# Kernel tuning notes

Hardware: AMD Instinct MI355X
Metric: run time of the kernel (lower is better)

The kernel has to match this reference:

```python
import jax, jax.numpy as jnp
import numpy as np

B, T, D, K = 8, 2048, 768, 2048

def setup_inputs() -> dict:
    key = jax.random.key(0)
    k1, k2 = jax.random.split(key)
    token = jax.random.normal(k1, (B, T, D), dtype=jnp.float32)
    codebook = jax.random.normal(k2, (K, D), dtype=jnp.float32)
    return {"token": token, "codebook": codebook}

def reference(token, codebook):
    x_sq = jnp.sum(token * token, axis=-1, keepdims=True)          # [B,T,1]
    e_sq = jnp.sum(codebook * codebook, axis=-1)                   # [K]
    dots = jnp.einsum('btd,kd->btk', token, codebook)              # [B,T,K]
    dist = x_sq - 2.0 * dots + e_sq                                # [B,T,K]
    indices = jnp.argmin(dist, axis=-1)                            # [B,T] int
    quantize = codebook[indices]                                   # [B,T,D] gather
    # commitment loss: mse(sg(quantize), x)
    commit_loss = jnp.mean(jnp.square(jax.lax.stop_gradient(quantize) - token))
    # straight-through estimator
    quantized = token + jax.lax.stop_gradient(quantize - token)
    return quantized, indices, commit_loss
```

## Files before the change

kernel.cpp:

```cpp
#include <hip/hip_runtime.h>

#define M_TOK 16384
#define D_DIM 768
#define K_CB  2048

#define BTOK  128
#define BCODE 128
#define BK    32
#define KSPLIT 8
#define SLICE (K_CB / KSPLIT)
#define NCT   (SLICE / BCODE)
#define NSLOT (KSPLIT * 2)
#define EPS   0.25f

typedef __attribute__((ext_vector_type(8))) short bf16x8;
typedef __attribute__((ext_vector_type(4))) float f32x4;

__device__ __forceinline__ unsigned short f2bf(float x) {
    unsigned u = __float_as_uint(x);
    return (unsigned short)((u + 0x7fffu + ((u >> 16) & 1u)) >> 16);
}
__device__ __forceinline__ float bf2f(unsigned short h) {
    return __uint_as_float((unsigned)h << 16);
}

#define ASYNC16(gp, lp) __builtin_amdgcn_global_load_lds( \
    (const __attribute__((address_space(1))) void*)(gp),  \
    (__attribute__((address_space(3))) void*)(lp), 16, 0, 0)

__global__ void vq_prep_cb(const float* __restrict__ cb,
                           unsigned short* __restrict__ cb_hi,
                           unsigned short* __restrict__ cb_lo,
                           float* __restrict__ esq) {
    const int w = threadIdx.x >> 6, lane = threadIdx.x & 63;
    const int k = blockIdx.x * 4 + w;
    const float* row = cb + (size_t)k * D_DIM;
    unsigned short* hk = cb_hi + (size_t)k * D_DIM;
    unsigned short* lk = cb_lo + (size_t)k * D_DIM;
    float s = 0.f;
    for (int j = lane; j < D_DIM; j += 64) {
        float x = row[j];
        s = fmaf(x, x, s);
        unsigned short h = f2bf(x);
        hk[j] = h;
        lk[j] = f2bf(x - bf2f(h));
    }
    #pragma unroll
    for (int off = 32; off; off >>= 1) s += __shfl_down(s, off);
    if (!lane) esq[k] = s;
}

__global__ void vq_prep_tok(const float* __restrict__ tok,
                            unsigned short* __restrict__ th,
                            unsigned short* __restrict__ tl) {
    const int N8 = (M_TOK * D_DIM) / 8;
    const int stride = gridDim.x * blockDim.x;
    for (int i = blockIdx.x * blockDim.x + threadIdx.x; i < N8; i += stride) {
        const float4 a = *(const float4*)(tok + (size_t)i * 8);
        const float4 b = *(const float4*)(tok + (size_t)i * 8 + 4);
        const float v[8] = {a.x, a.y, a.z, a.w, b.x, b.y, b.z, b.w};
        unsigned hh[8], ll[8];
        #pragma unroll
        for (int j = 0; j < 8; ++j) {
            const unsigned short h = f2bf(v[j]);
            hh[j] = h;
            ll[j] = f2bf(v[j] - bf2f(h));
        }
        uint4 ph, pl;
        ph.x = hh[0] | (hh[1] << 16);  ph.y = hh[2] | (hh[3] << 16);
        ph.z = hh[4] | (hh[5] << 16);  ph.w = hh[6] | (hh[7] << 16);
        pl.x = ll[0] | (ll[1] << 16);  pl.y = ll[2] | (ll[3] << 16);
        pl.z = ll[4] | (ll[5] << 16);  pl.w = ll[6] | (ll[7] << 16);
        *(uint4*)(th + (size_t)i * 8) = ph;
        *(uint4*)(tl + (size_t)i * 8) = pl;
    }
}

__launch_bounds__(256, 4)
__global__ void vq_dist_mfma(const unsigned short* __restrict__ tok_hi,
                             const unsigned short* __restrict__ tok_lo,
                             const unsigned short* __restrict__ cb_hi,
                             const unsigned short* __restrict__ cb_lo,
                             const float* __restrict__ esq,
                             float4* __restrict__ top2) {
    __shared__ unsigned short sAh[BCODE * BK];
    __shared__ unsigned short sAl[BCODE * BK];
    __shared__ unsigned short sBh[BTOK * BK];
    __shared__ unsigned short sBl[BTOK * BK];
    __shared__ float esq_s[SLICE];

    const int tid  = threadIdx.x;
    const int lane = tid & 63;
    const int w    = tid >> 6;

    const int bid = blockIdx.x;
    const int ksl = bid & 7;
    const int txi = bid >> 3;
    const int tokBase    = txi * BTOK;
    const int kSliceBase = ksl * SLICE;

    for (int j = tid; j < SLICE; j += 256) esq_s[j] = esq[kSliceBase + j];

    int gOff[2], gLds[2];
    #pragma unroll
    for (int q = 0; q < 2; ++q) {
        const int G   = w * 128 + q * 64 + lane;
        const int row = G >> 2;
        const int hs  = (G & 3) ^ ((row >> 1) & 3);
        gOff[q] = (row * D_DIM + hs * 8) * 2;
        gLds[q] = G * 16;
    }

    const int h  = lane >> 4;
    const int lm = lane & 15;
    const int wc = (w >> 1) * 64;
    const int wt = (w & 1) * 64;
    int offA[4], offB[4];
    #pragma unroll
    for (int i = 0; i < 4; ++i) {
        const int rA = wc + i * 16 + lm;
        offA[i] = rA * 64 + ((h ^ ((rA >> 1) & 3)) * 16);
        const int rB = wt + i * 16 + lm;
        offB[i] = rB * 64 + ((h ^ ((rB >> 1) & 3)) * 16);
    }

    float rm1[4], rm2[4];
    int   rk1[4], rk2[4];
    #pragma unroll
    for (int j = 0; j < 4; ++j) {
        rm1[j] = 3.4e38f; rm2[j] = 3.4e38f;
        rk1[j] = 0x7fffffff; rk2[j] = 0x7fffffff;
    }

    const char* pBh = (const char*)(tok_hi + (size_t)tokBase * D_DIM);
    const char* pBl = (const char*)(tok_lo + (size_t)tokBase * D_DIM);

    for (int ct = 0; ct < NCT; ++ct) {
        const int codeBase = kSliceBase + ct * BCODE;
        const char* pAh = (const char*)(cb_hi + (size_t)codeBase * D_DIM);
        const char* pAl = (const char*)(cb_lo + (size_t)codeBase * D_DIM);

        f32x4 acc[4][4];
        #pragma unroll
        for (int i = 0; i < 4; ++i)
            #pragma unroll
            for (int j = 0; j < 4; ++j) acc[i][j] = (f32x4){0.f, 0.f, 0.f, 0.f};

        for (int dc = 0; dc < D_DIM; dc += BK) {
            const int dcb = dc * 2;
            __syncthreads();
            #pragma unroll
            for (int q = 0; q < 2; ++q) {
                ASYNC16(pAh + gOff[q] + dcb, (char*)sAh + gLds[q]);
                ASYNC16(pAl + gOff[q] + dcb, (char*)sAl + gLds[q]);
                ASYNC16(pBh + gOff[q] + dcb, (char*)sBh + gLds[q]);
                ASYNC16(pBl + gOff[q] + dcb, (char*)sBl + gLds[q]);
            }
            __syncthreads();

            bf16x8 ah[4], al[4], bh[4], bl[4];
            #pragma unroll
            for (int i = 0; i < 4; ++i) {
                ah[i] = *(const bf16x8*)((const char*)sAh + offA[i]);
                al[i] = *(const bf16x8*)((const char*)sAl + offA[i]);
            }
            #pragma unroll
            for (int j = 0; j < 4; ++j) {
                bh[j] = *(const bf16x8*)((const char*)sBh + offB[j]);
                bl[j] = *(const bf16x8*)((const char*)sBl + offB[j]);
            }
            #pragma unroll
            for (int i = 0; i < 4; ++i)
                #pragma unroll
                for (int j = 0; j < 4; ++j) {
                    acc[i][j] = __builtin_amdgcn_mfma_f32_16x16x32_bf16(ah[i], bh[j], acc[i][j], 0, 0, 0);
                    acc[i][j] = __builtin_amdgcn_mfma_f32_16x16x32_bf16(ah[i], bl[j], acc[i][j], 0, 0, 0);
                    acc[i][j] = __builtin_amdgcn_mfma_f32_16x16x32_bf16(al[i], bh[j], acc[i][j], 0, 0, 0);
                }
        }

        #pragma unroll
        for (int j = 0; j < 4; ++j)
            #pragma unroll
            for (int i = 0; i < 4; ++i)
                #pragma unroll
                for (int r = 0; r < 4; ++r) {
                    const int cl = ct * BCODE + wc + i * 16 + (lane >> 4) * 4 + r;
                    const float s = esq_s[cl] - 2.0f * acc[i][j][r];
                    const int kg = kSliceBase + cl;
                    if (s < rm1[j]) {
                        rm2[j] = rm1[j]; rk2[j] = rk1[j];
                        rm1[j] = s;      rk1[j] = kg;
                    } else if (s < rm2[j]) {
                        rm2[j] = s; rk2[j] = kg;
                    }
                }
    }

    #pragma unroll
    for (int j = 0; j < 4; ++j) {
        float m1 = rm1[j], m2 = rm2[j];
        int   k1 = rk1[j], k2 = rk2[j];
        #pragma unroll
        for (int off = 16; off <= 32; off <<= 1) {
            const float om1 = __shfl_xor(m1, off); const int ok1 = __shfl_xor(k1, off);
            const float om2 = __shfl_xor(m2, off); const int ok2 = __shfl_xor(k2, off);
            const bool aB = (m1 < om1) || (m1 == om1 && k1 < ok1);
            float n1m, n2m; int n1k, n2k;
            if (aB) {
                n1m = m1; n1k = k1;
                const bool t = (om1 < m2) || (om1 == m2 && ok1 < k2);
                n2m = t ? om1 : m2; n2k = t ? ok1 : k2;
            } else {
                n1m = om1; n1k = ok1;
                const bool t = (m1 < om2) || (m1 == om2 && k1 < ok2);
                n2m = t ? m1 : om2; n2k = t ? k1 : ok2;
            }
            m1 = n1m; k1 = n1k; m2 = n2m; k2 = n2k;
        }
        if (lane < 16) {
            const int t = tokBase + wt + j * 16 + lane;
            const int slot = ksl * 2 + (w >> 1);
            top2[(size_t)t * NSLOT + slot] =
                make_float4(m1, __int_as_float(k1), m2, __int_as_float(k2));
        }
    }
}

__global__ void vq_final(const float* __restrict__ token,
                         const float* __restrict__ cb,
                         const float* __restrict__ esq,
                         const float4* __restrict__ top2,
                         float* __restrict__ out_q,
                         float* __restrict__ out_idx,
                         float* __restrict__ out_loss) {
    const int w = threadIdx.x >> 6, lane = threadIdx.x & 63;
    const int t = blockIdx.x * 4 + w;

    const float4 sv = top2[(size_t)t * NSLOT + (lane & 15)];
    float m1 = sv.x, m2 = sv.z;
    int   k1 = __float_as_int(sv.y), k2 = __float_as_int(sv.w);
    #pragma unroll
    for (int off = 1; off <= 8; off <<= 1) {
        const float om1 = __shfl_xor(m1, off); const int ok1 = __shfl_xor(k1, off);
        const float om2 = __shfl_xor(m2, off); const int ok2 = __shfl_xor(k2, off);
        const bool aB = (m1 < om1) || (m1 == om1 && k1 < ok1);
        float n1m, n2m; int n1k, n2k;
        if (aB) {
            n1m = m1; n1k = k1;
            const bool c = (om1 < m2) || (om1 == m2 && ok1 < k2);
            n2m = c ? om1 : m2; n2k = c ? ok1 : k2;
        } else {
            n1m = om1; n1k = ok1;
            const bool c = (m1 < om2) || (m1 == om2 && k1 < ok2);
            n2m = c ? m1 : om2; n2k = c ? k1 : ok2;
        }
        m1 = n1m; k1 = n1k; m2 = n2m; k2 = n2k;
    }

    unsigned choice = (unsigned)k1;
    if (!(m2 - m1 > EPS)) {
        const float* tr = token + (size_t)t * D_DIM;
        const float* c1 = cb + (size_t)k1 * D_DIM;
        const float* c2 = cb + (size_t)k2 * D_DIM;
        float d1 = 0.f, d2 = 0.f;
        for (int e = lane; e < D_DIM; e += 64) {
            const float x = tr[e];
            d1 = fmaf(c1[e], x, d1);
            d2 = fmaf(c2[e], x, d2);
        }
        #pragma unroll
        for (int off = 32; off; off >>= 1) {
            d1 += __shfl_down(d1, off);
            d2 += __shfl_down(d2, off);
        }
        d1 = __shfl(d1, 0);
        d2 = __shfl(d2, 0);
        const float s1 = esq[k1] - 2.f * d1;
        const float s2 = esq[k2] - 2.f * d2;
        if (s2 < s1 || (s2 == s1 && k2 < k1)) choice = (unsigned)k2;
    }

    const float* crow = cb + (size_t)choice * D_DIM;
    const float* trow = token + (size_t)t * D_DIM;
    float*       qrow = out_q + (size_t)t * D_DIM;
    float lsum = 0.f;
    #pragma unroll
    for (int u = 0; u < 3; ++u) {
        const int e = (u * 64 + lane) * 4;
        const float4 q = *(const float4*)(crow + e);
        const float4 x = *(const float4*)(trow + e);
        *(float4*)(qrow + e) = q;
        const float dx = q.x - x.x, dy = q.y - x.y, dz = q.z - x.z, dw = q.w - x.w;
        lsum += dx * dx + dy * dy + dz * dz + dw * dw;
    }
    if (!lane) out_idx[t] = (float)choice;

    #pragma unroll
    for (int off = 32; off; off >>= 1) lsum += __shfl_down(lsum, off);
    __shared__ float ws4[4];
    if (!lane) ws4[w] = lsum;
    __syncthreads();
    if (!threadIdx.x)
        atomicAdd(out_loss, (ws4[0] + ws4[1] + ws4[2] + ws4[3]) *
                            (1.0f / (float)((size_t)M_TOK * D_DIM)));
}

extern "C" void kernel_launch(void* const* d_in, const int* in_sizes, int n_in,
                              void* d_out, int out_size, void* d_ws, size_t ws_size,
                              hipStream_t stream) {
    const float* token = (const float*)d_in[0];
    const float* cb    = (const float*)d_in[1];

    float* out_q    = (float*)d_out;
    float* out_idx  = out_q + (size_t)M_TOK * D_DIM;
    float* out_loss = out_idx + M_TOK;

    unsigned short* tok_hi = (unsigned short*)out_q;
    unsigned short* tok_lo = tok_hi + (size_t)M_TOK * D_DIM;

    char* ws = (char*)d_ws;
    unsigned short* cb_hi = (unsigned short*)(ws);
    unsigned short* cb_lo = (unsigned short*)(ws + 3145728);
    float*          esq   = (float*)(ws + 6291456);
    float4*         top2  = (float4*)(ws + 6299648);

    hipMemsetAsync(out_loss, 0, sizeof(float), stream);

    vq_prep_cb<<<K_CB / 4, 256, 0, stream>>>(cb, cb_hi, cb_lo, esq);
    vq_prep_tok<<<3072, 256, 0, stream>>>(token, tok_hi, tok_lo);

    vq_dist_mfma<<<(M_TOK / BTOK) * KSPLIT, 256, 0, stream>>>(
        tok_hi, tok_lo, cb_hi, cb_lo, esq, top2);

    vq_final<<<M_TOK / 4, 256, 0, stream>>>(token, cb, esq, top2,
                                            out_q, out_idx, out_loss);
}
```

Baseline: 348.1 us.

## Retile distance GEMM to 64x512 blocks with XCD-aware mapping, merge prep kernels

Restructures the distance kernel so each 512-thread block handles 64 tokens against a 512-code slice in one pass, instead of 128 tokens looping over 128-code tiles. Block indices are mapped so blocks on the same XCD share a codebook slice, aiming to improve L2 reuse of the codebook. The two prep kernels are merged into one launch to cut launch overhead. The tradeoff is higher LDS and register use per block from the larger A tile and 8x2 accumulators, which may limit occupancy.

```diff
diff --git a/kernel.cpp b/kernel.cpp
--- a/kernel.cpp
+++ b/kernel.cpp
@@ -4,13 +4,12 @@
 #define D_DIM 768
 #define K_CB  2048
 
-#define BTOK  128
-#define BCODE 128
+#define BTOK  64
+#define BCODE 512
 #define BK    32
-#define KSPLIT 8
-#define SLICE (K_CB / KSPLIT)
-#define NCT   (SLICE / BCODE)
-#define NSLOT (KSPLIT * 2)
+#define KSPLIT 4
+#define NT    (D_DIM / BK)
+#define NSLOT 16
 #define EPS   0.25f
 
 typedef __attribute__((ext_vector_type(8))) short bf16x8;
@@ -28,179 +27,171 @@
     (const __attribute__((address_space(1))) void*)(gp),  \
     (__attribute__((address_space(3))) void*)(lp), 16, 0, 0)
 
-__global__ void vq_prep_cb(const float* __restrict__ cb,
-                           unsigned short* __restrict__ cb_hi,
-                           unsigned short* __restrict__ cb_lo,
-                           float* __restrict__ esq) {
-    const int w = threadIdx.x >> 6, lane = threadIdx.x & 63;
-    const int k = blockIdx.x * 4 + w;
-    const float* row = cb + (size_t)k * D_DIM;
-    unsigned short* hk = cb_hi + (size_t)k * D_DIM;
-    unsigned short* lk = cb_lo + (size_t)k * D_DIM;
-    float s = 0.f;
-    for (int j = lane; j < D_DIM; j += 64) {
-        float x = row[j];
-        s = fmaf(x, x, s);
-        unsigned short h = f2bf(x);
-        hk[j] = h;
-        lk[j] = f2bf(x - bf2f(h));
-    }
-    #pragma unroll
-    for (int off = 32; off; off >>= 1) s += __shfl_down(s, off);
-    if (!lane) esq[k] = s;
-}
-
-__global__ void vq_prep_tok(const float* __restrict__ tok,
-                            unsigned short* __restrict__ th,
-                            unsigned short* __restrict__ tl) {
-    const int N8 = (M_TOK * D_DIM) / 8;
-    const int stride = gridDim.x * blockDim.x;
-    for (int i = blockIdx.x * blockDim.x + threadIdx.x; i < N8; i += stride) {
-        const float4 a = *(const float4*)(tok + (size_t)i * 8);
-        const float4 b = *(const float4*)(tok + (size_t)i * 8 + 4);
-        const float v[8] = {a.x, a.y, a.z, a.w, b.x, b.y, b.z, b.w};
-        unsigned hh[8], ll[8];
-        #pragma unroll
-        for (int j = 0; j < 8; ++j) {
-            const unsigned short h = f2bf(v[j]);
-            hh[j] = h;
-            ll[j] = f2bf(v[j] - bf2f(h));
-        }
-        uint4 ph, pl;
-        ph.x = hh[0] | (hh[1] << 16);  ph.y = hh[2] | (hh[3] << 16);
-        ph.z = hh[4] | (hh[5] << 16);  ph.w = hh[6] | (hh[7] << 16);
-        pl.x = ll[0] | (ll[1] << 16);  pl.y = ll[2] | (ll[3] << 16);
-        pl.z = ll[4] | (ll[5] << 16);  pl.w = ll[6] | (ll[7] << 16);
-        *(uint4*)(th + (size_t)i * 8) = ph;
-        *(uint4*)(tl + (size_t)i * 8) = pl;
-    }
-}
-
-__launch_bounds__(256, 4)
-__global__ void vq_dist_mfma(const unsigned short* __restrict__ tok_hi,
-                             const unsigned short* __restrict__ tok_lo,
-                             const unsigned short* __restrict__ cb_hi,
-                             const unsigned short* __restrict__ cb_lo,
-                             const float* __restrict__ esq,
-                             float4* __restrict__ top2) {
+__global__ void vq_prep(const float* __restrict__ cb,
+                        const float* __restrict__ tok,
+                        unsigned short* __restrict__ cb_hi,
+                        unsigned short* __restrict__ cb_lo,
+                        float* __restrict__ esq,
+                        unsigned short* __restrict__ tok_hi,
+                        unsigned short* __restrict__ tok_lo) {
+    const int bid = blockIdx.x;
+    if (bid < 512) {
+        const int w = threadIdx.x >> 6, lane = threadIdx.x & 63;
+        const int k = bid * 4 + w;
+        const float* row = cb + (size_t)k * D_DIM;
+        unsigned short* hk = cb_hi + (size_t)k * D_DIM;
+        unsigned short* lk = cb_lo + (size_t)k * D_DIM;
+        float s = 0.f;
+        for (int j = lane; j < D_DIM; j += 64) {
+            float x = row[j];
+            s = fmaf(x, x, s);
+            unsigned short h = f2bf(x);
+            hk[j] = h;
+            lk[j] = f2bf(x - bf2f(h));
+        }
+        #pragma unroll
+        for (int off = 32; off; off >>= 1) s += __shfl_down(s, off);
+        if (!lane) esq[k] = s;
+    } else {
+        const int N8 = (M_TOK * D_DIM) / 8;
+        const int stride = 256 * 256;
+        for (int i = (bid - 512) * 256 + threadIdx.x; i < N8; i += stride) {
+            const float4 a = *(const float4*)(tok + (size_t)i * 8);
+            const float4 b = *(const float4*)(tok + (size_t)i * 8 + 4);
+            const float v[8] = {a.x, a.y, a.z, a.w, b.x, b.y, b.z, b.w};
+            unsigned hh[8], ll[8];
+            #pragma unroll
+            for (int j = 0; j < 8; ++j) {
+                const unsigned short h = f2bf(v[j]);
+                hh[j] = h;
+                ll[j] = f2bf(v[j] - bf2f(h));
+            }
+            uint4 ph, pl;
+            ph.x = hh[0] | (hh[1] << 16);  ph.y = hh[2] | (hh[3] << 16);
+            ph.z = hh[4] | (hh[5] << 16);  ph.w = hh[6] | (hh[7] << 16);
+            pl.x = ll[0] | (ll[1] << 16);  pl.y = ll[2] | (ll[3] << 16);
+            pl.z = ll[4] | (ll[5] << 16);  pl.w = ll[6] | (ll[7] << 16);
+            *(uint4*)(tok_hi + (size_t)i * 8) = ph;
+            *(uint4*)(tok_lo + (size_t)i * 8) = pl;
+        }
+    }
+}
+
+__launch_bounds__(512, 4)
+__global__ void vq_dist(const unsigned short* __restrict__ tok_hi,
+                        const unsigned short* __restrict__ tok_lo,
+                        const unsigned short* __restrict__ cb_hi,
+                        const unsigned short* __restrict__ cb_lo,
+                        const float* __restrict__ esq,
+                        float4* __restrict__ top2) {
     __shared__ unsigned short sAh[BCODE * BK];
     __shared__ unsigned short sAl[BCODE * BK];
     __shared__ unsigned short sBh[BTOK * BK];
     __shared__ unsigned short sBl[BTOK * BK];
-    __shared__ float esq_s[SLICE];
+    __shared__ float sE[BCODE];
 
     const int tid  = threadIdx.x;
     const int lane = tid & 63;
     const int w    = tid >> 6;
 
     const int bid = blockIdx.x;
-    const int ksl = bid & 7;
-    const int txi = bid >> 3;
-    const int tokBase    = txi * BTOK;
-    const int kSliceBase = ksl * SLICE;
-
-    for (int j = tid; j < SLICE; j += 256) esq_s[j] = esq[kSliceBase + j];
-
-    int gOff[2], gLds[2];
-    #pragma unroll
-    for (int q = 0; q < 2; ++q) {
-        const int G   = w * 128 + q * 64 + lane;
+    const int xcd = bid & 7;
+    const int m   = bid >> 3;
+    const int ksl = xcd >> 1;
+    const int txi = m | ((xcd & 1) << 7);
+    const int tokBase = txi * BTOK;
+    const int kBase   = ksl * BCODE;
+
+    for (int j = tid; j < BCODE; j += 512) sE[j] = esq[kBase + j];
+
+    int gOffA[4], ldsA[4];
+    #pragma unroll
+    for (int q = 0; q < 4; ++q) {
+        const int G   = q * 512 + tid;
         const int row = G >> 2;
-        const int hs  = (G & 3) ^ ((row >> 1) & 3);
-        gOff[q] = (row * D_DIM + hs * 8) * 2;
-        gLds[q] = G * 16;
-    }
+        const int sl  = (G & 3) ^ ((row >> 1) & 3);
+        gOffA[q] = row * D_DIM + sl * 8;
+        ldsA[q]  = G * 16;
+    }
+    const int gB   = tid & 255;
+    const int rowB = gB >> 2;
+    const int slB  = (gB & 3) ^ ((rowB >> 1) & 3);
+    const int gOffB = rowB * D_DIM + slB * 8;
+    const int ldsB  = gB * 16;
+
+    const unsigned short* pAh = cb_hi + (size_t)kBase * D_DIM;
+    const unsigned short* pAl = cb_lo + (size_t)kBase * D_DIM;
+    const unsigned short* pBsel = ((tid < 256) ? tok_hi : tok_lo)
+                                  + (size_t)tokBase * D_DIM;
+    char* sBsel = (tid < 256) ? (char*)sBh : (char*)sBl;
 
     const int h  = lane >> 4;
     const int lm = lane & 15;
-    const int wc = (w >> 1) * 64;
-    const int wt = (w & 1) * 64;
-    int offA[4], offB[4];
-    #pragma unroll
-    for (int i = 0; i < 4; ++i) {
+    const int wr = w >> 1;
+    const int wc = wr * 128;
+    const int wt = (w & 1) * 32;
+    int offA[8], offB[2];
+    #pragma unroll
+    for (int i = 0; i < 8; ++i) {
         const int rA = wc + i * 16 + lm;
         offA[i] = rA * 64 + ((h ^ ((rA >> 1) & 3)) * 16);
-        const int rB = wt + i * 16 + lm;
-        offB[i] = rB * 64 + ((h ^ ((rB >> 1) & 3)) * 16);
-    }
-
-    float rm1[4], rm2[4];
-    int   rk1[4], rk2[4];
-    #pragma unroll
-    for (int j = 0; j < 4; ++j) {
-        rm1[j] = 3.4e38f; rm2[j] = 3.4e38f;
-        rk1[j] = 0x7fffffff; rk2[j] = 0x7fffffff;
-    }
-
-    const char* pBh = (const char*)(tok_hi + (size_t)tokBase * D_DIM);
-    const char* pBl = (const char*)(tok_lo + (size_t)tokBase * D_DIM);
-
-    for (int ct = 0; ct < NCT; ++ct) {
-        const int codeBase = kSliceBase + ct * BCODE;
-        const char* pAh = (const char*)(cb_hi + (size_t)codeBase * D_DIM);
-        const char* pAl = (const char*)(cb_lo + (size_t)codeBase * D_DIM);
-
-        f32x4 acc[4][4];
-        #pragma unroll
-        for (int i = 0; i < 4; ++i)
+    }
+    #pragma unroll
+    for (int j = 0; j < 2; ++j) {
+        const int rB = wt + j * 16 + lm;
+        offB[j] = rB * 64 + ((h ^ ((rB >> 1) & 3)) * 16);
+    }
+
+    f32x4 acc[8][2];
+    #pragma unroll
+    for (int i = 0; i < 8; ++i)
+        #pragma unroll
+        for (int j = 0; j < 2; ++j) acc[i][j] = (f32x4){0.f, 0.f, 0.f, 0.f};
+
+    for (int t = 0; t < NT; ++t) {
+        const int dco = t * BK;
+        __syncthreads();
+        #pragma unroll
+        for (int q = 0; q < 4; ++q) {
+            ASYNC16(pAh + gOffA[q] + dco, (char*)sAh + ldsA[q]);
+            ASYNC16(pAl + gOffA[q] + dco, (char*)sAl + ldsA[q]);
+        }
+        ASYNC16(pBsel + gOffB + dco, sBsel + ldsB);
+        __syncthreads();
+
+        bf16x8 bh[2], bl[2];
+        #pragma unroll
+        for (int j = 0; j < 2; ++j) {
+            bh[j] = *(const bf16x8*)((const char*)sBh + offB[j]);
+            bl[j] = *(const bf16x8*)((const char*)sBl + offB[j]);
+        }
+        #pragma unroll
+        for (int i = 0; i < 8; ++i) {
+            const bf16x8 ah = *(const bf16x8*)((const char*)sAh + offA[i]);
+            acc[i][0] = __builtin_amdgcn_mfma_f32_16x16x32_bf16(ah, bh[0], acc[i][0], 0, 0, 0);
+            acc[i][1] = __builtin_amdgcn_mfma_f32_16x16x32_bf16(ah, bh[1], acc[i][1], 0, 0, 0);
+            acc[i][0] = __builtin_amdgcn_mfma_f32_16x16x32_bf16(ah, bl[0], acc[i][0], 0, 0, 0);
+            acc[i][1] = __builtin_amdgcn_mfma_f32_16x16x32_bf16(ah, bl[1], acc[i][1], 0, 0, 0);
+            const bf16x8 al = *(const bf16x8*)((const char*)sAl + offA[i]);
+            acc[i][0] = __builtin_amdgcn_mfma_f32_16x16x32_bf16(al, bh[0], acc[i][0], 0, 0, 0);
+            acc[i][1] = __builtin_amdgcn_mfma_f32_16x16x32_bf16(al, bh[1], acc[i][1], 0, 0, 0);
+        }
+    }
+
+    #pragma unroll
+    for (int j = 0; j < 2; ++j) {
+        float m1 = 3.4e38f, m2 = 3.4e38f;
+        int   k1 = 0x7fffffff, k2 = 0x7fffffff;
+        #pragma unroll
+        for (int i = 0; i < 8; ++i)
             #pragma unroll
-            for (int j = 0; j < 4; ++j) acc[i][j] = (f32x4){0.f, 0.f, 0.f, 0.f};
-
-        for (int dc = 0; dc < D_DIM; dc += BK) {
-            const int dcb = dc * 2;
-            __syncthreads();
-            #pragma unroll
-            for (int q = 0; q < 2; ++q) {
-                ASYNC16(pAh + gOff[q] + dcb, (char*)sAh + gLds[q]);
-                ASYNC16(pAl + gOff[q] + dcb, (char*)sAl + gLds[q]);
-                ASYNC16(pBh + gOff[q] + dcb, (char*)sBh + gLds[q]);
-                ASYNC16(pBl + gOff[q] + dcb, (char*)sBl + gLds[q]);
+            for (int r = 0; r < 4; ++r) {
+                const int cl = wc + i * 16 + (lane >> 4) * 4 + r;
+                const float s = sE[cl] - 2.0f * acc[i][j][r];
+                const int kg = kBase + cl;
+                if (s < m1)      { m2 = m1; k2 = k1; m1 = s; k1 = kg; }
+                else if (s < m2) { m2 = s; k2 = kg; }
             }
-            __syncthreads();
-
-            bf16x8 ah[4], al[4], bh[4], bl[4];
-            #pragma unroll
-            for (int i = 0; i < 4; ++i) {
-                ah[i] = *(const bf16x8*)((const char*)sAh + offA[i]);
-                al[i] = *(const bf16x8*)((const char*)sAl + offA[i]);
-            }
-            #pragma unroll
-            for (int j = 0; j < 4; ++j) {
-                bh[j] = *(const bf16x8*)((const char*)sBh + offB[j]);
-                bl[j] = *(const bf16x8*)((const char*)sBl + offB[j]);
-            }
-            #pragma unroll
-            for (int i = 0; i < 4; ++i)
-                #pragma unroll
-                for (int j = 0; j < 4; ++j) {
-                    acc[i][j] = __builtin_amdgcn_mfma_f32_16x16x32_bf16(ah[i], bh[j], acc[i][j], 0, 0, 0);
-                    acc[i][j] = __builtin_amdgcn_mfma_f32_16x16x32_bf16(ah[i], bl[j], acc[i][j], 0, 0, 0);
-                    acc[i][j] = __builtin_amdgcn_mfma_f32_16x16x32_bf16(al[i], bh[j], acc[i][j], 0, 0, 0);
-                }
-        }
-
-        #pragma unroll
-        for (int j = 0; j < 4; ++j)
-            #pragma unroll
-            for (int i = 0; i < 4; ++i)
-                #pragma unroll
-                for (int r = 0; r < 4; ++r) {
-                    const int cl = ct * BCODE + wc + i * 16 + (lane >> 4) * 4 + r;
-                    const float s = esq_s[cl] - 2.0f * acc[i][j][r];
-                    const int kg = kSliceBase + cl;
-                    if (s < rm1[j]) {
-                        rm2[j] = rm1[j]; rk2[j] = rk1[j];
-                        rm1[j] = s;      rk1[j] = kg;
-                    } else if (s < rm2[j]) {
-                        rm2[j] = s; rk2[j] = kg;
-                    }
-                }
-    }
-
-    #pragma unroll
-    for (int j = 0; j < 4; ++j) {
-        float m1 = rm1[j], m2 = rm2[j];
-        int   k1 = rk1[j], k2 = rk2[j];
         #pragma unroll
         for (int off = 16; off <= 32; off <<= 1) {
             const float om1 = __shfl_xor(m1, off); const int ok1 = __shfl_xor(k1, off);
@@ -209,19 +200,18 @@
             float n1m, n2m; int n1k, n2k;
             if (aB) {
                 n1m = m1; n1k = k1;
-                const bool t = (om1 < m2) || (om1 == m2 && ok1 < k2);
-                n2m = t ? om1 : m2; n2k = t ? ok1 : k2;
+                const bool c = (om1 < m2) || (om1 == m2 && ok1 < k2);
+                n2m = c ? om1 : m2; n2k = c ? ok1 : k2;
             } else {
                 n1m = om1; n1k = ok1;
-                const bool t = (m1 < om2) || (m1 == om2 && k1 < ok2);
-                n2m = t ? m1 : om2; n2k = t ? k1 : ok2;
+                const bool c = (m1 < om2) || (m1 == om2 && k1 < ok2);
+                n2m = c ? m1 : om2; n2k = c ? k1 : ok2;
             }
             m1 = n1m; k1 = n1k; m2 = n2m; k2 = n2k;
         }
         if (lane < 16) {
-            const int t = tokBase + wt + j * 16 + lane;
-            const int slot = ksl * 2 + (w >> 1);
-            top2[(size_t)t * NSLOT + slot] =
+            const int tt = tokBase + wt + j * 16 + lane;
+            top2[(size_t)tt * NSLOT + (ksl * 4 + wr)] =
                 make_float4(m1, __int_as_float(k1), m2, __int_as_float(k2));
         }
     }
@@ -327,10 +317,10 @@
 
     hipMemsetAsync(out_loss, 0, sizeof(float), stream);
 
-    vq_prep_cb<<<K_CB / 4, 256, 0, stream>>>(cb, cb_hi, cb_lo, esq);
-    vq_prep_tok<<<3072, 256, 0, stream>>>(token, tok_hi, tok_lo);
-
-    vq_dist_mfma<<<(M_TOK / BTOK) * KSPLIT, 256, 0, stream>>>(
+    vq_prep<<<768, 256, 0, stream>>>(cb, token, cb_hi, cb_lo, esq,
+                                     tok_hi, tok_lo);
+
+    vq_dist<<<(M_TOK / BTOK) * KSPLIT, 512, 0, stream>>>(
         tok_hi, tok_lo, cb_hi, cb_lo, esq, top2);
 
     vq_final<<<M_TOK / 4, 256, 0, stream>>>(token, cb, esq, top2,
```

Measured after the change: 331.3 us. -4.8%, faster.
